# Performance work log

Measured on AMD Instinct MI355X. Metric: run time of the kernel, lower is better.

## Reference

```python
import jax, jax.numpy as jnp
import numpy as np

B, T, N, D, H = 2, 12, 1024, 128, 8
HD = D // H  # head_dim = 16


def setup_inputs() -> dict:
    key = jax.random.key(0)
    ks = jax.random.split(key, 11)
    std = 0.02
    return {
        "query": jax.random.normal(ks[0], (B, T, N, D), dtype=jnp.float32),
        "key": jax.random.normal(ks[1], (B, T, N, D), dtype=jnp.float32),
        "value": jax.random.normal(ks[2], (B, T, N, D), dtype=jnp.float32),
        "Wq": jax.random.normal(ks[3], (D, D), dtype=jnp.float32) * std,
        "bq": jnp.zeros((D,), dtype=jnp.float32),
        "Wk": jax.random.normal(ks[4], (D, D), dtype=jnp.float32) * std,
        "bk": jnp.zeros((D,), dtype=jnp.float32),
        "Wv": jax.random.normal(ks[5], (D, D), dtype=jnp.float32) * std,
        "bv": jnp.zeros((D,), dtype=jnp.float32),
        "Wo": jax.random.normal(ks[6], (D, D), dtype=jnp.float32) * std,
        "bo": jnp.zeros((D,), dtype=jnp.float32),
    }


def reference(query, key, value, Wq, bq, Wk, bk, Wv, bv, Wo, bo):
    # Linear projections (torch nn.Linear: x @ W.T + b)
    q = query @ Wq.T + bq   # (B,T,N,D)
    k = key @ Wk.T + bk
    v = value @ Wv.T + bv
    # split heads: last dim D -> (H, HD)
    q = q.reshape(B, T, N, H, HD)
    k = k.reshape(B, T, N, H, HD)
    v = v.reshape(B, T, N, H, HD)
    scale = 1.0 / jnp.sqrt(jnp.float32(HD))
    # attention across node dim (N); scores (B,H,T,N,N) ~ 805 MB
    scores = jnp.einsum('btnhd,btmhd->bhtnm', q, k) * scale
    attn = jax.nn.softmax(scores, axis=-1)
    out = jnp.einsum('bhtnm,btmhd->btnhd', attn, v)  # (B,T,N,H,HD)
    out = out.reshape(B, T, N, D)
    return out @ Wo.T + bo
```

## Files before the change

kernel.cpp:

```cpp
#include <hip/hip_runtime.h>


#define DEV __device__ __forceinline__

typedef __attribute__((ext_vector_type(4))) float f32x4;
typedef __attribute__((ext_vector_type(16))) float f32x16;
typedef __attribute__((ext_vector_type(8))) short s16x8;
typedef __attribute__((ext_vector_type(4))) short s16x4;
typedef __attribute__((ext_vector_type(2))) unsigned int u32x2;
typedef __attribute__((ext_vector_type(4))) unsigned int u32x4;

DEV unsigned short f2bf(float f) {
    unsigned u = __builtin_bit_cast(unsigned, f);
    u = (u + 0x7fffu + ((u >> 16) & 1u)) >> 16;
    return (unsigned short)u;
}

DEV unsigned pack_bf16(float a, float b) {
    unsigned ua = __builtin_bit_cast(unsigned, a) + 0x8000u;
    unsigned ub = __builtin_bit_cast(unsigned, b) + 0x8000u;
    return __builtin_amdgcn_perm(ub, ua, 0x07060302);
}

DEV f32x16 mfma3216(s16x8 a, s16x8 b, f32x16 c) {
    return __builtin_amdgcn_mfma_f32_32x32x16_bf16(a, b, c, 0, 0, 0);
}

__global__ __launch_bounds__(256)
void qkv_proj_kernel(const float* __restrict__ xq, const float* __restrict__ xk,
                     const float* __restrict__ xv,
                     const float* __restrict__ Wq, const float* __restrict__ Wk,
                     const float* __restrict__ Wv,
                     const float* __restrict__ bq, const float* __restrict__ bk,
                     const float* __restrict__ bv,
                     unsigned short* __restrict__ oq, unsigned short* __restrict__ ok,
                     unsigned short* __restrict__ ov)
{
    const int z = blockIdx.y;
    const float* X    = (z == 0) ? xq : (z == 1) ? xk : xv;
    const float* W    = (z == 0) ? Wq : (z == 1) ? Wk : Wv;
    const float* bias = (z == 0) ? bq : (z == 1) ? bk : bv;
    unsigned short* out = (z == 0) ? oq : (z == 1) ? ok : ov;
    const float scale = (z == 0) ? 0.25f * 1.44269504088896f : 1.0f;

    __shared__ unsigned short Xs[64 * 136];
    __shared__ unsigned short Ws[128 * 136];

    const int t  = threadIdx.x;
    const int m0 = blockIdx.x * 64;

    {
        const float4* Xg = (const float4*)(X + (size_t)m0 * 128);
        #pragma unroll
        for (int p = 0; p < 8; p++) {
            int g = p * 256 + t;
            float4 vv = Xg[g];
            int row = g >> 5, c4 = g & 31;
            ushort4 d;
            d.x = f2bf(vv.x); d.y = f2bf(vv.y); d.z = f2bf(vv.z); d.w = f2bf(vv.w);
            *(ushort4*)&Xs[row * 136 + c4 * 4] = d;
        }
        const float4* Wg = (const float4*)W;
        #pragma unroll
        for (int p = 0; p < 16; p++) {
            int g = p * 256 + t;
            float4 vv = Wg[g];
            int row = g >> 5, c4 = g & 31;
            ushort4 d;
            d.x = f2bf(vv.x); d.y = f2bf(vv.y); d.z = f2bf(vv.z); d.w = f2bf(vv.w);
            *(ushort4*)&Ws[row * 136 + c4 * 4] = d;
        }
    }
    __syncthreads();

    const int wave = t >> 6, lane = t & 63, quad = lane >> 4, n16 = lane & 15;
    f32x4 acc[8];
    const f32x4 zero4 = {0.f, 0.f, 0.f, 0.f};
    #pragma unroll
    for (int i = 0; i < 8; i++) acc[i] = zero4;

    #pragma unroll
    for (int ks = 0; ks < 4; ks++) {
        s16x8 a = *(const s16x8*)&Xs[(wave * 16 + n16) * 136 + ks * 32 + quad * 8];
        #pragma unroll
        for (int nt = 0; nt < 8; nt++) {
            s16x8 b = *(const s16x8*)&Ws[(nt * 16 + n16) * 136 + ks * 32 + quad * 8];
            acc[nt] = __builtin_amdgcn_mfma_f32_16x16x32_bf16(a, b, acc[nt], 0, 0, 0);
        }
    }

    const int bt    = m0 >> 10;
    const int nbase = (m0 & 1023) + wave * 16 + quad * 4;
    if (z == 2) {
        #pragma unroll
        for (int nt = 0; nt < 8; nt++) {
            float bb = bias[nt * 16 + n16];
            u32x2 pv = {pack_bf16(acc[nt][0] + bb, acc[nt][1] + bb),
                        pack_bf16(acc[nt][2] + bb, acc[nt][3] + bb)};
            *(u32x2*)&out[((size_t)(bt * 8 + nt) * 16 + n16) * 1024 + nbase] = pv;
        }
    } else {
        __syncthreads();
        const int crow = wave * 16 + quad * 4;
        #pragma unroll
        for (int nt = 0; nt < 8; nt++) {
            float bb = bias[nt * 16 + n16];
            #pragma unroll
            for (int r = 0; r < 4; r++)
                Xs[(crow + r) * 136 + nt * 16 + n16] = f2bf((acc[nt][r] + bb) * scale);
        }
        __syncthreads();
        #pragma unroll
        for (int p = 0; p < 4; p++) {
            int g = p * 256 + t, row = g >> 4, ch = g & 15;
            s16x8 val = *(const s16x8*)&Xs[row * 136 + ch * 8];
            *(s16x8*)&out[((size_t)(bt * 8 + (ch >> 1)) * 1024 + (m0 & 1023) + row) * 16
                          + (ch & 1) * 8] = val;
        }
    }
}

__global__ __launch_bounds__(256, 6)
void attn_kernel(const unsigned short* __restrict__ q,
                 const unsigned short* __restrict__ k,
                 const unsigned short* __restrict__ vt,
                 unsigned short* __restrict__ O)
{
    __shared__ unsigned char smem[8192 + 2 * 5712];

    const int t    = threadIdx.x;
    const int lane = t & 63;
    const int wave = t >> 6;
    const int hi   = lane >> 5;
    const int l31  = lane & 31;
    const int h = blockIdx.x, bx = blockIdx.y, bt = blockIdx.z;
    const size_t headoff = (size_t)(bt * 8 + h) * 16384;

    const int q0 = bx * 128 + wave * 32;

    s16x8 qf = *(const s16x8*)(q + headoff + (size_t)(q0 + l31) * 16 + hi * 8);

    const int krow = t >> 1, kss = t & 1;
    const int kj   = krow & 31;
    const int km   = (kj & ~12) | ((kj & 4) << 1) | ((kj & 8) >> 1);
    const unsigned kdst = (unsigned)((krow >> 5) * 1024 + kss * 512 + km * 16);
    const unsigned short* kg = k + headoff + (size_t)krow * 16 + kss * 8;
    const int vrow = t >> 4, vjb = t & 15;
    const unsigned vdst = (unsigned)(8192 + vrow * 272 + vjb * 16);
    const unsigned short* vg = vt + headoff + (size_t)vrow * 1024 + vjb * 8;

    const unsigned krd = (unsigned)(lane * 16);
    const int vr = (l31 > 20) ? 20 : l31;
    const unsigned vrd = (unsigned)(8192 + vr * 272 + hi * 16);

    for (int idx = t; idx < 640; idx += 256) {
        int b = idx / 320, rem = idx - b * 320;
        int row = 16 + (rem >> 6), col = rem & 63;
        unsigned val = (row == 16 || row == 20) ? 0x3F803F80u : 0u;
        *(unsigned*)&smem[8192 + b * 5712 + row * 272 + col * 4] = val;
    }

    {
        s16x8 kv = *(const s16x8*)kg;
        s16x8 vv = *(const s16x8*)vg;
        *(s16x8*)&smem[kdst] = kv;
        *(s16x8*)&smem[vdst] = vv;
    }

    f32x16 acc;
    #pragma unroll
    for (int i = 0; i < 16; i++) acc[i] = 0.f;
    f32x16 zero16;
    #pragma unroll
    for (int i = 0; i < 16; i++) zero16[i] = 0.f;

    #pragma unroll
    for (int c = 0; c < 8; c++) {
        __syncthreads();
        s16x8 kv, vv;
        if (c < 7) {
            kv = *(const s16x8*)(kg + (size_t)(c + 1) * 2048);
            vv = *(const s16x8*)(vg + (size_t)(c + 1) * 128);
        }
        const unsigned kb = krd + (c & 1) * 4096;
        const unsigned vb = vrd + (c & 1) * 5712;
        #pragma unroll
        for (int w = 0; w < 4; w++) {
            s16x8 ka = *(const s16x8*)&smem[kb + w * 1024];
            f32x16 s = mfma3216(ka, qf, zero16);
            float p[16];
            #pragma unroll
            for (int i = 0; i < 16; i++) p[i] = __builtin_amdgcn_exp2f(s[i]);
            u32x4 pa0 = {pack_bf16(p[0],  p[1]),  pack_bf16(p[2],  p[3]),
                         pack_bf16(p[4],  p[5]),  pack_bf16(p[6],  p[7])};
            u32x4 pa1 = {pack_bf16(p[8],  p[9]),  pack_bf16(p[10], p[11]),
                         pack_bf16(p[12], p[13]), pack_bf16(p[14], p[15])};
            s16x8 vf0 = *(const s16x8*)&smem[vb + w * 64];
            s16x8 vf1 = *(const s16x8*)&smem[vb + w * 64 + 32];
            acc = mfma3216(vf0, __builtin_bit_cast(s16x8, pa0), acc);
            acc = mfma3216(vf1, __builtin_bit_cast(s16x8, pa1), acc);
        }
        if (c < 7) {
            *(s16x8*)&smem[kdst + (((c + 1) & 1) ? 4096u : 0u)] = kv;
            *(s16x8*)&smem[vdst + (((c + 1) & 1) ? 5712u : 0u)] = vv;
        }
    }

    float dinv = __builtin_amdgcn_rcpf(acc[8]);
    __syncthreads();
    const unsigned ob = (unsigned)((wave * 32 + l31) * 40);
    u32x2 w0 = { pack_bf16(acc[0] * dinv, acc[1] * dinv),
                 pack_bf16(acc[2] * dinv, acc[3] * dinv) };
    u32x2 w1 = { pack_bf16(acc[4] * dinv, acc[5] * dinv),
                 pack_bf16(acc[6] * dinv, acc[7] * dinv) };
    *(u32x2*)&smem[ob + hi * 8]      = w0;
    *(u32x2*)&smem[ob + 16 + hi * 8] = w1;
    __syncthreads();
    {
        int qq = t >> 1, half = t & 1;
        s16x8 ov = *(const s16x8*)&smem[qq * 40 + half * 16];
        *(s16x8*)&O[((size_t)bt * 1024 + bx * 128 + qq) * 128 + h * 16 + half * 8] = ov;
    }
}

__global__ __launch_bounds__(256)
void o_proj_kernel(const unsigned short* __restrict__ X, const float* __restrict__ W,
                   const float* __restrict__ bias, float* __restrict__ out)
{
    __shared__ unsigned short Xs[64 * 136];
    __shared__ unsigned short Ws[128 * 136];

    const int t  = threadIdx.x;
    const int m0 = blockIdx.x * 64;

    {
        #pragma unroll
        for (int p = 0; p < 4; p++) {
            int g = p * 256 + t, row = g >> 4, ch = g & 15;
            *(s16x8*)&Xs[row * 136 + ch * 8] =
                *(const s16x8*)(X + (size_t)(m0 + row) * 128 + ch * 8);
        }
        const float4* Wg = (const float4*)W;
        #pragma unroll
        for (int p = 0; p < 16; p++) {
            int g = p * 256 + t;
            float4 vv = Wg[g];
            int row = g >> 5, c4 = g & 31;
            ushort4 d;
            d.x = f2bf(vv.x); d.y = f2bf(vv.y); d.z = f2bf(vv.z); d.w = f2bf(vv.w);
            *(ushort4*)&Ws[row * 136 + c4 * 4] = d;
        }
    }
    __syncthreads();

    const int wave = t >> 6, lane = t & 63, quad = lane >> 4, n16 = lane & 15;
    f32x4 acc[8];
    const f32x4 zero4 = {0.f, 0.f, 0.f, 0.f};
    #pragma unroll
    for (int i = 0; i < 8; i++) acc[i] = zero4;

    #pragma unroll
    for (int ks = 0; ks < 4; ks++) {
        s16x8 a = *(const s16x8*)&Xs[(wave * 16 + n16) * 136 + ks * 32 + quad * 8];
        #pragma unroll
        for (int nt = 0; nt < 8; nt++) {
            s16x8 b = *(const s16x8*)&Ws[(nt * 16 + n16) * 136 + ks * 32 + quad * 8];
            acc[nt] = __builtin_amdgcn_mfma_f32_16x16x32_bf16(a, b, acc[nt], 0, 0, 0);
        }
    }

    const int mrow = m0 + wave * 16 + quad * 4;
    #pragma unroll
    for (int nt = 0; nt < 8; nt++) {
        float bb = bias[nt * 16 + n16];
        #pragma unroll
        for (int r = 0; r < 4; r++)
            out[(size_t)(mrow + r) * 128 + nt * 16 + n16] = acc[nt][r] + bb;
    }
}

extern "C" void kernel_launch(void* const* d_in, const int* in_sizes, int n_in,
                              void* d_out, int out_size, void* d_ws, size_t ws_size,
                              hipStream_t stream)
{
    const float* query = (const float*)d_in[0];
    const float* key_  = (const float*)d_in[1];
    const float* value = (const float*)d_in[2];
    const float* Wq = (const float*)d_in[3];
    const float* bq = (const float*)d_in[4];
    const float* Wk = (const float*)d_in[5];
    const float* bk = (const float*)d_in[6];
    const float* Wv = (const float*)d_in[7];
    const float* bv = (const float*)d_in[8];
    const float* Wo = (const float*)d_in[9];
    const float* bo = (const float*)d_in[10];
    float* out = (float*)d_out;

    char* ws = (char*)d_ws;
    unsigned short* qb = (unsigned short*)(ws);
    unsigned short* kb = (unsigned short*)(ws + 6291456);
    unsigned short* vb = (unsigned short*)(ws + 12582912);
    unsigned short* Ob = (unsigned short*)(ws + 18874368);

    qkv_proj_kernel<<<dim3(384, 3, 1), 256, 0, stream>>>(
        query, key_, value, Wq, Wk, Wv, bq, bk, bv, qb, kb, vb);
    attn_kernel<<<dim3(8, 8, 24), 256, 0, stream>>>(qb, kb, vb, Ob);
    o_proj_kernel<<<dim3(384, 1, 1), 256, 0, stream>>>(Ob, Wo, bo, out);
}
```

Before: 139.5 us.

## Stream K/V tiles into LDS with direct global-to-LDS loads and swizzled V layout

Replaces the register-staged double buffer for K and V in the attention kernel with `global_load_lds` 16-byte transfers that write straight into shared memory. The V tile now uses an XOR-swizzled, unpadded layout, and the padded ones-rows that formed the softmax denominator become a single 64-byte ones row. This removes the per-chunk VGPR staging, the separate LDS store instructions and the padding initialisation, and it shrinks the LDS footprint. In exchange it depends on the compiler placing correct vmcnt waits before each barrier for the asynchronous LDS writes, and on the swizzled addressing staying free of bank conflicts.

```diff
diff --git a/kernel.cpp b/kernel.cpp
--- a/kernel.cpp
+++ b/kernel.cpp
@@ -24,6 +24,12 @@
 
 DEV f32x16 mfma3216(s16x8 a, s16x8 b, f32x16 c) {
     return __builtin_amdgcn_mfma_f32_32x32x16_bf16(a, b, c, 0, 0, 0);
+}
+
+DEV void gload16(const unsigned short* g, unsigned short* l) {
+    __builtin_amdgcn_global_load_lds(
+        (const __attribute__((address_space(1))) unsigned int*)g,
+        (__attribute__((address_space(3))) unsigned int*)l, 16, 0, 0);
 }
 
 __global__ __launch_bounds__(256)
@@ -126,7 +132,7 @@
                  const unsigned short* __restrict__ vt,
                  unsigned short* __restrict__ O)
 {
-    __shared__ unsigned char smem[8192 + 2 * 5712];
+    __shared__ unsigned char smem[16448];
 
     const int t    = threadIdx.x;
     const int lane = t & 63;
@@ -140,32 +146,22 @@
 
     s16x8 qf = *(const s16x8*)(q + headoff + (size_t)(q0 + l31) * 16 + hi * 8);
 
-    const int krow = t >> 1, kss = t & 1;
-    const int kj   = krow & 31;
-    const int km   = (kj & ~12) | ((kj & 4) << 1) | ((kj & 8) >> 1);
-    const unsigned kdst = (unsigned)((krow >> 5) * 1024 + kss * 512 + km * 16);
-    const unsigned short* kg = k + headoff + (size_t)krow * 16 + kss * 8;
-    const int vrow = t >> 4, vjb = t & 15;
-    const unsigned vdst = (unsigned)(8192 + vrow * 272 + vjb * 16);
-    const unsigned short* vg = vt + headoff + (size_t)vrow * 1024 + vjb * 8;
-
-    const unsigned krd = (unsigned)(lane * 16);
-    const int vr = (l31 > 20) ? 20 : l31;
-    const unsigned vrd = (unsigned)(8192 + vr * 272 + hi * 16);
-
-    for (int idx = t; idx < 640; idx += 256) {
-        int b = idx / 320, rem = idx - b * 320;
-        int row = 16 + (rem >> 6), col = rem & 63;
-        unsigned val = (row == 16 || row == 20) ? 0x3F803F80u : 0u;
-        *(unsigned*)&smem[8192 + b * 5712 + row * 272 + col * 4] = val;
-    }
-
-    {
-        s16x8 kv = *(const s16x8*)kg;
-        s16x8 vv = *(const s16x8*)vg;
-        *(s16x8*)&smem[kdst] = kv;
-        *(s16x8*)&smem[vdst] = vv;
-    }
+    if (t < 16) *(unsigned*)&smem[16384 + t * 4] = 0x3F803F80u;
+
+    const int km_ = lane & 31;
+    const int kpi = (km_ & ~12) | ((km_ & 4) << 1) | ((km_ & 8) >> 1);
+    const unsigned short* kg =
+        k + headoff + (size_t)(wave * 32 + kpi) * 16 + (lane >> 5) * 8;
+    const int vm_ = t >> 4;
+    const int vo_ = (t & 15) ^ (vm_ & 7);
+    const unsigned short* vg = vt + headoff + (size_t)vm_ * 1024 + vo_ * 8;
+    const unsigned kdst = (unsigned)(wave * 1024 + lane * 16);
+    const unsigned vdst = (unsigned)(8192 + wave * 1024 + lane * 16);
+
+    const unsigned vrow = (l31 < 16) ? (unsigned)(l31 * 256) : 0xFFFFFFFFu;
+
+    gload16(kg, (unsigned short*)&smem[kdst]);
+    gload16(vg, (unsigned short*)&smem[vdst]);
 
     f32x16 acc;
     #pragma unroll
@@ -177,32 +173,32 @@
     #pragma unroll
     for (int c = 0; c < 8; c++) {
         __syncthreads();
-        s16x8 kv, vv;
         if (c < 7) {
-            kv = *(const s16x8*)(kg + (size_t)(c + 1) * 2048);
-            vv = *(const s16x8*)(vg + (size_t)(c + 1) * 128);
-        }
-        const unsigned kb = krd + (c & 1) * 4096;
-        const unsigned vb = vrd + (c & 1) * 5712;
+            unsigned nb = ((c + 1) & 1) ? 4096u : 0u;
+            gload16(kg + (size_t)(c + 1) * 2048, (unsigned short*)&smem[kdst + nb]);
+            gload16(vg + (size_t)(c + 1) * 128,  (unsigned short*)&smem[vdst + nb]);
+        }
+        const unsigned kb  = (unsigned)((c & 1) * 4096) + (unsigned)(lane * 16);
+        const unsigned vb0 = 8192u + (unsigned)((c & 1) * 4096);
         #pragma unroll
         for (int w = 0; w < 4; w++) {
             s16x8 ka = *(const s16x8*)&smem[kb + w * 1024];
             f32x16 s = mfma3216(ka, qf, zero16);
-            float p[16];
+            u32x4 pa0, pa1;
             #pragma unroll
-            for (int i = 0; i < 16; i++) p[i] = __builtin_amdgcn_exp2f(s[i]);
-            u32x4 pa0 = {pack_bf16(p[0],  p[1]),  pack_bf16(p[2],  p[3]),
-                         pack_bf16(p[4],  p[5]),  pack_bf16(p[6],  p[7])};
-            u32x4 pa1 = {pack_bf16(p[8],  p[9]),  pack_bf16(p[10], p[11]),
-                         pack_bf16(p[12], p[13]), pack_bf16(p[14], p[15])};
-            s16x8 vf0 = *(const s16x8*)&smem[vb + w * 64];
-            s16x8 vf1 = *(const s16x8*)&smem[vb + w * 64 + 32];
+            for (int i = 0; i < 4; i++) {
+                pa0[i] = pack_bf16(__builtin_amdgcn_exp2f(s[2 * i]),
+                                   __builtin_amdgcn_exp2f(s[2 * i + 1]));
+                pa1[i] = pack_bf16(__builtin_amdgcn_exp2f(s[8 + 2 * i]),
+                                   __builtin_amdgcn_exp2f(s[8 + 2 * i + 1]));
+            }
+            unsigned vaddr = (vrow == 0xFFFFFFFFu)
+                ? 16384u
+                : vb0 + vrow + (unsigned)(((((w << 2) + hi) ^ (l31 & 7))) << 4);
+            s16x8 vf0 = *(const s16x8*)&smem[vaddr];
+            s16x8 vf1 = *(const s16x8*)&smem[vaddr ^ 32u];
             acc = mfma3216(vf0, __builtin_bit_cast(s16x8, pa0), acc);
             acc = mfma3216(vf1, __builtin_bit_cast(s16x8, pa1), acc);
-        }
-        if (c < 7) {
-            *(s16x8*)&smem[kdst + (((c + 1) & 1) ? 4096u : 0u)] = kv;
-            *(s16x8*)&smem[vdst + (((c + 1) & 1) ? 5712u : 0u)] = vv;
         }
     }
 
```

Result: no change. 137.8 us (-1.3%).
